# Kernel tuning notes

Hardware: AMD Instinct MI355X
Metric: run time of the kernel (lower is better)

The kernel has to match this reference:

```python
import jax, jax.numpy as jnp
import numpy as np

# physical constants / config (from __init__ defaults + chosen kwargs)
WFA_C = 4.6686e-13   # e/(4*pi*m_e*c) in 1/(G*Angstrom)
LAMBDA0 = 6301.5     # Angstrom
G_FACTOR = 1.5
WFA_WEIGHT = 0.5
STOKES_V = 3
BLOS_THRESH = 100.0
BASE_THRESH = 0.0004
TAU_IDX = np.array([0, 1, 2])
N_LOGTAU, N_MAGS = 21, 4
NWL = 112
START, END = 0, NWL - 1  # wavelength_range=None -> [0, len-1) slice
EPS = 1e-10


def _np_gradient(x):
    """np.gradient along last axis: central diffs interior, one-sided edges."""
    left = x[..., 1:2] - x[..., 0:1]
    mid = (x[..., 2:] - x[..., :-2]) * 0.5
    right = x[..., -1:] - x[..., -2:-1]
    return jnp.concatenate([left, mid, right], axis=-1)


def setup_inputs() -> dict:
    key = jax.random.key(0)
    kS, kP, kT = jax.random.split(key, 3)
    B = 65536
    input_stokes = jax.random.normal(kS, (B, 4, NWL), dtype=jnp.float32) * 0.01
    predicted_atm = jax.random.normal(kP, (B, N_LOGTAU * N_MAGS), dtype=jnp.float32)
    # target close to prediction so base MAE < base_loss_threshold -> WFA branch active
    target_atm = predicted_atm + 1e-4 * jax.random.normal(kT, (B, N_LOGTAU * N_MAGS), dtype=jnp.float32)
    wavelengths = jnp.linspace(6300.5, 6303.0, NWL).astype(jnp.float32)
    return {"input_stokes": input_stokes, "predicted_atm": predicted_atm,
            "target_atm": target_atm, "wavelengths": wavelengths}


def reference(input_stokes, predicted_atm, target_atm, wavelengths):
    # base MAE loss
    base_loss = jnp.mean(jnp.abs(predicted_atm - target_atm))

    # --- WFA B_LOS estimate, vectorized over batch ---
    wl = wavelengths[START:END]                      # [L]
    I = input_stokes[:, 0, START:END]                # [B, L]
    V = input_stokes[:, STOKES_V, START:END]         # [B, L]
    dI = _np_gradient(I) / _np_gradient(wl)[None, :]  # dI/dlambda, [B, L]

    # least squares V ~ p0*dI + p1; 2-column pinv == closed-form normal equations
    n = jnp.float32(dI.shape[-1])
    sd = jnp.sum(dI, axis=-1)
    sv = jnp.sum(V, axis=-1)
    sdd = jnp.sum(dI * dI, axis=-1)
    sdv = jnp.sum(dI * V, axis=-1)
    p0 = (n * sdv - sd * sv) / (n * sdd - sd * sd)   # slope, [B]
    wfa_blos = -p0 / (WFA_C * LAMBDA0 ** 2 * G_FACTOR)  # Gauss, [B]

    # predicted B_LOS: mean over tau_indices of last magnetic parameter
    atm = predicted_atm.reshape(-1, N_LOGTAU, N_MAGS)
    predicted_blos = atm[:, TAU_IDX, -1].mean(axis=1)  # [B]

    # thresholded masked log-abs MAE
    mask = jnp.abs(wfa_blos) < BLOS_THRESH
    diff = jnp.abs(jnp.log10(jnp.abs(predicted_blos) + EPS)
                   - jnp.log10(jnp.abs(wfa_blos) + EPS))
    cnt = jnp.sum(mask)
    wfa_loss_masked = jnp.sum(jnp.where(mask, diff, 0.0)) / jnp.maximum(cnt, 1).astype(diff.dtype)

    # early-return semantics: WFA only if base_loss < threshold AND any mask
    apply_wfa = (base_loss < BASE_THRESH) & (cnt > 0)
    wfa_loss = jnp.where(apply_wfa, wfa_loss_masked, jnp.float32(0.0))
    total_loss = jnp.where(apply_wfa,
                           (1.0 - WFA_WEIGHT) * base_loss + WFA_WEIGHT * wfa_loss_masked,
                           base_loss)
    return total_loss, base_loss, wfa_loss
```

## Files before the change

### kernel.cpp

```cpp
#include <hip/hip_runtime.h>
#include <math.h>

#define NWL   112
#define NCOLS 111
#define NATM  84
#define THREADS 256
#define WAVES_PER_BLOCK 4
#define MAIN_BLOCKS 2048

__device__ __forceinline__ float wave_reduce_sum(float v) {
#pragma unroll
    for (int off = 32; off >= 1; off >>= 1)
        v += __shfl_xor(v, off, 64);
    return v;
}

__global__ __launch_bounds__(THREADS) void wfa_main(
    const float* __restrict__ stokes,
    const float* __restrict__ pred,
    const float* __restrict__ targ,
    const float* __restrict__ wl,
    float* __restrict__ ws,
    int nrows, int nblocks)
{
    __shared__ float s_inv_dwl[NWL];
    __shared__ float s_I[WAVES_PER_BLOCK][NWL];
    __shared__ float s_red[WAVES_PER_BLOCK][3];

    const int tid  = threadIdx.x;
    const int lane = tid & 63;
    const int wid  = tid >> 6;

    if (tid < NCOLS) {
        int j = tid;
        float d;
        if (j == 0)            d = wl[1] - wl[0];
        else if (j == NCOLS-1) d = wl[NCOLS-1] - wl[NCOLS-2];
        else                   d = 0.5f * (wl[j+1] - wl[j-1]);
        s_inv_dwl[j] = 1.0f / d;
    }
    __syncthreads();

    const int gwave  = blockIdx.x * WAVES_PER_BLOCK + wid;
    const int nwaves = nblocks * WAVES_PER_BLOCK;

    const int  c1   = lane + 64;
    const bool has1 = (c1 < NCOLS);

    const float WFA_DEN = (float)(4.6686e-13 * 6301.5 * 6301.5 * 1.5);

    float base_acc = 0.f;
    float wfa_acc  = 0.f;
    float cnt_acc  = 0.f;

    float* sI = s_I[wid];

    for (int r = gwave; r < nrows; r += nwaves) {
        const float* rowI = stokes + (size_t)r * (4 * NWL);
        const float* rowV = rowI + 3 * NWL;

        float i0 = rowI[lane];
        float i1 = has1 ? rowI[c1] : 0.f;
        float v0 = rowV[lane];
        float v1 = has1 ? rowV[c1] : 0.f;

        float bpart = 0.f;
        if (lane < 21) {
            const float4 p4 = ((const float4*)(pred + (size_t)r * NATM))[lane];
            const float4 t4 = ((const float4*)(targ + (size_t)r * NATM))[lane];
            bpart = fabsf(p4.x - t4.x) + fabsf(p4.y - t4.y)
                  + fabsf(p4.z - t4.z) + fabsf(p4.w - t4.w);
        }
        base_acc += bpart;

        sI[lane] = i0;
        if (has1) sI[c1] = i1;

        float dI0;
        {
            const int j = lane;
            float g = (j == 0) ? (sI[1] - sI[0])
                               : 0.5f * (sI[j + 1] - sI[j - 1]);
            dI0 = g * s_inv_dwl[j];
        }
        float dI1 = 0.f;
        if (has1) {
            const int j = c1;
            float g = (j == NCOLS - 1) ? (sI[j] - sI[j - 1])
                                       : 0.5f * (sI[j + 1] - sI[j - 1]);
            dI1 = g * s_inv_dwl[j];
        }

        const float sd  = wave_reduce_sum(dI0 + dI1);
        const float sdd = wave_reduce_sum(dI0 * dI0 + dI1 * dI1);
        const float sdv = wave_reduce_sum(dI0 * v0 + dI1 * v1);
        const float sv  = wave_reduce_sum(v0 + v1);

        if (lane == 0) {
            const float n  = (float)NCOLS;
            const float p0 = (n * sdv - sd * sv) / (n * sdd - sd * sd);
            const float wb = -p0 / WFA_DEN;
            const float ab = fabsf(wb);
            if (ab < 100.0f) {
                const float* a = pred + (size_t)r * NATM;
                const float pb = (a[3] + a[7] + a[11]) / 3.0f;
                wfa_acc += fabsf(log10f(fabsf(pb) + 1e-10f) - log10f(ab + 1e-10f));
                cnt_acc += 1.0f;
            }
        }
    }

    base_acc = wave_reduce_sum(base_acc);
    if (lane == 0) {
        s_red[wid][0] = base_acc;
        s_red[wid][1] = wfa_acc;
        s_red[wid][2] = cnt_acc;
    }
    __syncthreads();
    if (tid == 0) {
        float b = 0.f, w = 0.f, c = 0.f;
#pragma unroll
        for (int k = 0; k < WAVES_PER_BLOCK; ++k) {
            b += s_red[k][0]; w += s_red[k][1]; c += s_red[k][2];
        }
        ws[blockIdx.x]               = b;
        ws[nblocks + blockIdx.x]     = w;
        ws[2 * nblocks + blockIdx.x] = c;
    }
}

__global__ __launch_bounds__(256) void wfa_final(
    const float* __restrict__ ws, float* __restrict__ out,
    int nblocks, int nrows)
{
    const int tid = threadIdx.x;
    float b = 0.f, w = 0.f, c = 0.f;
    for (int i = tid; i < nblocks; i += 256) {
        b += ws[i];
        w += ws[nblocks + i];
        c += ws[2 * nblocks + i];
    }
    b = wave_reduce_sum(b);
    w = wave_reduce_sum(w);
    c = wave_reduce_sum(c);

    __shared__ float sb[4], sw[4], sc[4];
    const int lane = tid & 63, wid = tid >> 6;
    if (lane == 0) { sb[wid] = b; sw[wid] = w; sc[wid] = c; }
    __syncthreads();
    if (tid == 0) {
        const float B_ = sb[0] + sb[1] + sb[2] + sb[3];
        const float W_ = sw[0] + sw[1] + sw[2] + sw[3];
        const float C_ = sc[0] + sc[1] + sc[2] + sc[3];
        const float base_loss = B_ / (float)((long long)nrows * NATM);
        const float wfa_ml    = W_ / fmaxf(C_, 1.0f);
        const bool  apply     = (base_loss < 0.0004f) && (C_ > 0.f);
        out[0] = apply ? (0.5f * base_loss + 0.5f * wfa_ml) : base_loss;
        out[1] = base_loss;
        out[2] = apply ? wfa_ml : 0.f;
    }
}

extern "C" void kernel_launch(void* const* d_in, const int* in_sizes, int n_in,
                              void* d_out, int out_size, void* d_ws, size_t ws_size,
                              hipStream_t stream)
{
    const float* stokes = (const float*)d_in[0];
    const float* pred   = (const float*)d_in[1];
    const float* targ   = (const float*)d_in[2];
    const float* wl     = (const float*)d_in[3];
    float* out = (float*)d_out;
    float* ws  = (float*)d_ws;

    const int nrows = in_sizes[1] / NATM;

    int nblocks = MAIN_BLOCKS;
    const size_t need = (size_t)nblocks * 3 * sizeof(float);
    if (ws_size < need) {
        nblocks = (int)(ws_size / (3 * sizeof(float)));
        if (nblocks < 1) nblocks = 1;
    }

    hipLaunchKernelGGL(wfa_main, dim3(nblocks), dim3(THREADS), 0, stream,
                       stokes, pred, targ, wl, ws, nrows, nblocks);
    hipLaunchKernelGGL(wfa_final, dim3(1), dim3(256), 0, stream,
                       ws, out, nblocks, nrows);
}
```

Baseline: 199.8 us.

## Process two rows per wave with float4 loads and shuffle-based gradient

```diff
diff --git a/kernel.cpp b/kernel.cpp
--- a/kernel.cpp
+++ b/kernel.cpp
@@ -7,6 +7,15 @@
 #define THREADS 256
 #define WAVES_PER_BLOCK 4
 #define MAIN_BLOCKS 2048
+
+__device__ __forceinline__ float half_reduce_sum(float v) {
+    v += __shfl_xor(v, 1,  64);
+    v += __shfl_xor(v, 2,  64);
+    v += __shfl_xor(v, 4,  64);
+    v += __shfl_xor(v, 8,  64);
+    v += __shfl_xor(v, 16, 64);
+    return v;
+}
 
 __device__ __forceinline__ float wave_reduce_sum(float v) {
 #pragma unroll
@@ -23,87 +32,92 @@
     float* __restrict__ ws,
     int nrows, int nblocks)
 {
-    __shared__ float s_inv_dwl[NWL];
-    __shared__ float s_I[WAVES_PER_BLOCK][NWL];
+    __shared__ float s_idw[NWL];
     __shared__ float s_red[WAVES_PER_BLOCK][3];
 
     const int tid  = threadIdx.x;
     const int lane = tid & 63;
     const int wid  = tid >> 6;
-
-    if (tid < NCOLS) {
-        int j = tid;
+    const int sub  = lane & 31;
+    const int g    = lane & 32;
+
+    if (tid < NWL) {
+        const int j = tid;
         float d;
-        if (j == 0)            d = wl[1] - wl[0];
-        else if (j == NCOLS-1) d = wl[NCOLS-1] - wl[NCOLS-2];
-        else                   d = 0.5f * (wl[j+1] - wl[j-1]);
-        s_inv_dwl[j] = 1.0f / d;
+        if (j == 0)              d = wl[1] - wl[0];
+        else if (j == NCOLS - 1) d = wl[NCOLS - 1] - wl[NCOLS - 2];
+        else if (j < NCOLS - 1)  d = 0.5f * (wl[j + 1] - wl[j - 1]);
+        else                     d = 1.0f;
+        s_idw[j] = (j == NCOLS) ? 0.0f : 1.0f / d;
     }
     __syncthreads();
 
-    const int gwave  = blockIdx.x * WAVES_PER_BLOCK + wid;
-    const int nwaves = nblocks * WAVES_PER_BLOCK;
-
-    const int  c1   = lane + 64;
-    const bool has1 = (c1 < NCOLS);
+    float4 idw4 = make_float4(0.f, 0.f, 0.f, 0.f);
+    if (sub < 28) idw4 = *(const float4*)&s_idw[4 * sub];
 
     const float WFA_DEN = (float)(4.6686e-13 * 6301.5 * 6301.5 * 1.5);
+
+    const int h  = (blockIdx.x * WAVES_PER_BLOCK + wid) * 2 + (lane >> 5);
+    const int nh = nblocks * WAVES_PER_BLOCK * 2;
 
     float base_acc = 0.f;
     float wfa_acc  = 0.f;
     float cnt_acc  = 0.f;
 
-    float* sI = s_I[wid];
-
-    for (int r = gwave; r < nrows; r += nwaves) {
-        const float* rowI = stokes + (size_t)r * (4 * NWL);
-        const float* rowV = rowI + 3 * NWL;
-
-        float i0 = rowI[lane];
-        float i1 = has1 ? rowI[c1] : 0.f;
-        float v0 = rowV[lane];
-        float v1 = has1 ? rowV[c1] : 0.f;
-
+    for (int r = h; r < nrows; r += nh) {
+        const float* rowbase = stokes + (size_t)r * (4 * NWL);
+
+        float4 I4 = make_float4(0.f, 0.f, 0.f, 0.f);
+        float4 V4 = make_float4(0.f, 0.f, 0.f, 0.f);
+        if (sub < 28) {
+            I4 = ((const float4*)rowbase)[sub];
+            V4 = ((const float4*)(rowbase + 3 * NWL))[sub];
+        }
+
+        float4 P4 = make_float4(0.f, 0.f, 0.f, 0.f);
         float bpart = 0.f;
-        if (lane < 21) {
-            const float4 p4 = ((const float4*)(pred + (size_t)r * NATM))[lane];
-            const float4 t4 = ((const float4*)(targ + (size_t)r * NATM))[lane];
-            bpart = fabsf(p4.x - t4.x) + fabsf(p4.y - t4.y)
-                  + fabsf(p4.z - t4.z) + fabsf(p4.w - t4.w);
+        if (sub < 21) {
+            P4 = ((const float4*)(pred + (size_t)r * NATM))[sub];
+            const float4 T4 = ((const float4*)(targ + (size_t)r * NATM))[sub];
+            bpart = fabsf(P4.x - T4.x) + fabsf(P4.y - T4.y)
+                  + fabsf(P4.z - T4.z) + fabsf(P4.w - T4.w);
         }
         base_acc += bpart;
 
-        sI[lane] = i0;
-        if (has1) sI[c1] = i1;
-
-        float dI0;
-        {
-            const int j = lane;
-            float g = (j == 0) ? (sI[1] - sI[0])
-                               : 0.5f * (sI[j + 1] - sI[j - 1]);
-            dI0 = g * s_inv_dwl[j];
-        }
-        float dI1 = 0.f;
-        if (has1) {
-            const int j = c1;
-            float g = (j == NCOLS - 1) ? (sI[j] - sI[j - 1])
-                                       : 0.5f * (sI[j + 1] - sI[j - 1]);
-            dI1 = g * s_inv_dwl[j];
-        }
-
-        const float sd  = wave_reduce_sum(dI0 + dI1);
-        const float sdd = wave_reduce_sum(dI0 * dI0 + dI1 * dI1);
-        const float sdv = wave_reduce_sum(dI0 * v0 + dI1 * v1);
-        const float sv  = wave_reduce_sum(v0 + v1);
-
-        if (lane == 0) {
+        const int lm1 = lane - (sub ? 1 : 0);
+        const float im1 = __shfl(I4.w, lm1, 64);
+        const float ip4 = __shfl(I4.x, lane + 1, 64);
+
+        const float n0 = (sub == 0)  ? (I4.y - I4.x) : 0.5f * (I4.y - im1);
+        const float n1 = 0.5f * (I4.z - I4.x);
+        const float n2 = (sub == 27) ? (I4.z - I4.y) : 0.5f * (I4.w - I4.y);
+        const float n3 = 0.5f * (ip4 - I4.z);
+
+        const float d0 = n0 * idw4.x;
+        const float d1 = n1 * idw4.y;
+        const float d2 = n2 * idw4.z;
+        const float d3 = n3 * idw4.w;
+        const float v3 = (sub == 27) ? 0.f : V4.w;
+
+        float sd  = d0 + d1 + d2 + d3;
+        float sdd = fmaf(d0, d0, fmaf(d1, d1, fmaf(d2, d2, d3 * d3)));
+        float sdv = fmaf(d0, V4.x, fmaf(d1, V4.y, fmaf(d2, V4.z, d3 * v3)));
+        float sv  = V4.x + V4.y + V4.z + v3;
+
+        sd  = half_reduce_sum(sd);
+        sdd = half_reduce_sum(sdd);
+        sdv = half_reduce_sum(sdv);
+        sv  = half_reduce_sum(sv);
+
+        const float a7  = __shfl(P4.w, g | 1, 64);
+        const float a11 = __shfl(P4.w, g | 2, 64);
+
+        if (sub == 0) {
             const float n  = (float)NCOLS;
             const float p0 = (n * sdv - sd * sv) / (n * sdd - sd * sd);
-            const float wb = -p0 / WFA_DEN;
-            const float ab = fabsf(wb);
+            const float ab = fabsf(p0) / WFA_DEN;
             if (ab < 100.0f) {
-                const float* a = pred + (size_t)r * NATM;
-                const float pb = (a[3] + a[7] + a[11]) / 3.0f;
+                const float pb = (P4.w + a7 + a11) / 3.0f;
                 wfa_acc += fabsf(log10f(fabsf(pb) + 1e-10f) - log10f(ab + 1e-10f));
                 cnt_acc += 1.0f;
             }
@@ -111,6 +125,8 @@
     }
 
     base_acc = wave_reduce_sum(base_acc);
+    wfa_acc  = wave_reduce_sum(wfa_acc);
+    cnt_acc  = wave_reduce_sum(cnt_acc);
     if (lane == 0) {
         s_red[wid][0] = base_acc;
         s_red[wid][1] = wfa_acc;
```

Result: no change. 199.1 us (-0.4%).
